# Optimization experiments

Measured on AMD Instinct MI355X. Metric: run time of the kernel, lower is better.

The kernel has to match this reference:

```python
import jax, jax.numpy as jnp
import numpy as np

N = 100000
E = 3200000
IN_C, HID, OUT_C = 512, 256, 40
NUM_LAYERS = 2
BN_EPS = 1e-5


def setup_inputs() -> dict:
    key = jax.random.key(0)
    ks = jax.random.split(key, 12)
    s = 0.05  # weight scale to keep activations sane
    return {
        "x": jax.random.normal(ks[0], (N, IN_C), jnp.float32),
        "edge_index": jax.random.randint(ks[1], (2, E), 0, N, jnp.int64),
        "fc0_W": jax.random.normal(ks[2], (IN_C, HID), jnp.float32) * s,
        "fc0_b": jax.random.normal(ks[3], (HID,), jnp.float32) * s,
        "conv_W": jax.random.normal(ks[4], (NUM_LAYERS, HID, HID), jnp.float32) * s,
        "conv_b": jax.random.normal(ks[5], (NUM_LAYERS, HID), jnp.float32) * s,
        "bn_gamma": jax.random.uniform(ks[6], (NUM_LAYERS + 1, HID), jnp.float32, 0.5, 1.5),
        "bn_beta": jax.random.normal(ks[7], (NUM_LAYERS + 1, HID), jnp.float32) * s,
        "bn_mean": jax.random.normal(ks[8], (NUM_LAYERS + 1, HID), jnp.float32) * s,
        "bn_var": jax.random.uniform(ks[9], (NUM_LAYERS + 1, HID), jnp.float32, 0.5, 1.5),
        "clf_W": jax.random.normal(ks[10], (HID, OUT_C), jnp.float32) * s,
        "clf_b": jax.random.normal(ks[11], (OUT_C,), jnp.float32) * s,
    }


def _bn(x, gamma, beta, mean, var):
    # BatchNorm1d in eval mode (running stats)
    return (x - mean) * (gamma * jax.lax.rsqrt(var + BN_EPS)) + beta


def _aggregate(x, row, col):
    # degree-normalized SpMM: out[col[e]] += (1/sqrt(d[col[e]]d[row[e]])) * x[row[e]]
    n = x.shape[0]
    d = jax.ops.segment_sum(jnp.ones((row.shape[0],), x.dtype), col, num_segments=n)
    dn = jnp.where(d > 0, jax.lax.rsqrt(d), 0.0)  # nan_to_num of 1/sqrt(0)
    val = dn[col] * dn[row]  # [E]
    msgs = val[:, None] * x[row]  # [E, HID]
    return jax.ops.segment_sum(msgs, col, num_segments=n)


def reference(x, edge_index, fc0_W, fc0_b, conv_W, conv_b,
              bn_gamma, bn_beta, bn_mean, bn_var, clf_W, clf_b):
    row, col = edge_index[0], edge_index[1]
    h = jax.nn.relu(_bn(x @ fc0_W + fc0_b, bn_gamma[0], bn_beta[0], bn_mean[0], bn_var[0]))
    prev = h  # layer_[-1] == layer_[0] (only one append)
    for i in range(NUM_LAYERS):
        h = _aggregate(h, row, col) @ conv_W[i] + conv_b[i]
        h = jax.nn.relu(_bn(h, bn_gamma[i + 1], bn_beta[i + 1], bn_mean[i + 1], bn_var[i + 1]))
        h = h + prev  # residual to first-layer features
    return h @ clf_W + clf_b
```

## Files before the change

kernel.cpp:

```cpp
#include <hip/hip_runtime.h>
#include <stdint.h>

#define NN 100000
#define NE 3200000
#define KIN 512
#define HID 256
#define NOUT 40
#define NB2 1024
#define BSHIFT2 7
#define NBKT 782
#define EPB 8192

typedef __attribute__((ext_vector_type(8))) __bf16 bf16x8;
typedef __attribute__((ext_vector_type(4))) float f32x4;

__device__ __forceinline__ float b2f(unsigned short u) {
  union { unsigned int i; float f; } x; x.i = ((unsigned int)u) << 16; return x.f;
}
__device__ __forceinline__ unsigned short f2b(float f) {
  unsigned int i = __float_as_uint(f);
  return (unsigned short)((i + 0x7FFFu + ((i >> 16) & 1u)) >> 16);
}
__device__ __forceinline__ float uf(unsigned int x) { return __uint_as_float(x); }
__device__ __forceinline__ unsigned char f2e8(float v) {
  v = fminf(v, 480.f);
  unsigned int ui = __float_as_uint(v);
  ui += 0x3FFFFu + ((ui >> 19) & 1u);
  unsigned int e32 = ui >> 23;
  if (e32 <= 120u) return 0;
  return (unsigned char)(((e32 - 120u) << 4) | ((ui >> 19) & 15u));
}
__device__ __forceinline__ float e82f(unsigned char u) {
  return __uint_as_float(((unsigned int)u) << 19) * 0x1p120f;
}
__device__ __forceinline__ unsigned short e82b(unsigned char u) {
  return u ? (unsigned short)(((unsigned int)u << 3) + 0x3C00u) : (unsigned short)0;
}
__device__ __forceinline__ unsigned short* swz(unsigned short* base, int row, int kk) {
  int byte = (row * 64 + kk * 2) ^ ((row & 7) << 4);
  return (unsigned short*)((char*)base + byte);
}
__device__ __forceinline__ char* swzst(unsigned short* base, int row, int cb) {
  int byte = (row * 128 + cb) ^ ((row & 7) << 4);
  return (char*)base + byte;
}

__global__ __launch_bounds__(256) void k_bhist(const int* __restrict__ ecol, int* __restrict__ bcnt) {
  __shared__ int hist[NB2];
  int t = threadIdx.x;
  for (int j = t; j < NB2; j += 256) hist[j] = 0;
  __syncthreads();
  int e0 = blockIdx.x * EPB, e1 = min(e0 + EPB, NE);
  for (int e = e0 + t; e < e1; e += 256) atomicAdd(&hist[ecol[e] >> BSHIFT2], 1);
  __syncthreads();
  for (int j = t; j < NB2; j += 256) if (hist[j]) atomicAdd(&bcnt[j], hist[j]);
}

__global__ void k_bscan(const int* __restrict__ bcnt, int* __restrict__ bbase, int* __restrict__ cursor) {
  __shared__ int wsum[4];
  int t = threadIdx.x, lane = t & 63, w = t >> 6;
  int4 v = *(const int4*)(bcnt + 4 * t);
  int tot = v.x + v.y + v.z + v.w;
  int s = tot;
  for (int d = 1; d < 64; d <<= 1) { int o = __shfl_up(s, d, 64); if (lane >= d) s += o; }
  if (lane == 63) wsum[w] = s;
  __syncthreads();
  int add = 0;
  for (int i = 0; i < 4; ++i) add += (i < w) ? wsum[i] : 0;
  int excl = add + s - tot;
  int p0 = excl, p1 = p0 + v.x, p2 = p1 + v.y, p3 = p2 + v.z;
  bbase[4 * t] = p0; bbase[4 * t + 1] = p1; bbase[4 * t + 2] = p2; bbase[4 * t + 3] = p3;
  cursor[4 * t] = p0; cursor[4 * t + 1] = p1; cursor[4 * t + 2] = p2; cursor[4 * t + 3] = p3;
}

__global__ __launch_bounds__(256) void k_bucket(const int* __restrict__ erow, const int* __restrict__ ecol,
                                                int* __restrict__ cursor, unsigned int* __restrict__ ebuf) {
  __shared__ int hist[NB2];
  __shared__ int base[NB2];
  int t = threadIdx.x;
  for (int j = t; j < NB2; j += 256) hist[j] = 0;
  __syncthreads();
  int e0 = blockIdx.x * EPB, e1 = min(e0 + EPB, NE);
  for (int e = e0 + t; e < e1; e += 256) atomicAdd(&hist[ecol[e] >> BSHIFT2], 1);
  __syncthreads();
  for (int j = t; j < NB2; j += 256) {
    int c = hist[j];
    base[j] = (c > 0) ? atomicAdd(&cursor[j], c) : 0;
    hist[j] = 0;
  }
  __syncthreads();
  for (int e = e0 + t; e < e1; e += 256) {
    int col = ecol[e];
    int b = col >> BSHIFT2;
    int r = atomicAdd(&hist[b], 1);
    ebuf[(size_t)base[b] + r] = ((unsigned int)(col & 127) << 17) | (unsigned int)erow[e];
  }
}

__global__ __launch_bounds__(256) void k_subdeg(const unsigned int* __restrict__ ebuf,
                                                const int* __restrict__ bbase, const int* __restrict__ bcnt,
                                                int* __restrict__ deg, float* __restrict__ dn) {
  __shared__ int h[128];
  int t = threadIdx.x, b = blockIdx.x;
  if (t < 128) h[t] = 0;
  __syncthreads();
  int s = bbase[b], e = s + bcnt[b];
  for (int i = s + t; i < e; i += 256) atomicAdd(&h[ebuf[i] >> 17], 1);
  __syncthreads();
  if (t < 128) {
    int col = (b << BSHIFT2) + t;
    if (col < NN) { int d = h[t]; deg[col] = d; dn[col] = d > 0 ? rsqrtf((float)d) : 0.f; }
  }
}

#define SCAN_CH 1024
__global__ void k_scan_part(const int* __restrict__ deg, int* __restrict__ partials) {
  __shared__ int lds[4];
  int b = blockIdx.x, t = threadIdx.x;
  int base = b * SCAN_CH;
  int s = 0;
  for (int j = 0; j < 4; ++j) { int i = base + t + 256 * j; if (i < NN) s += deg[i]; }
  for (int d = 32; d > 0; d >>= 1) s += __shfl_down(s, d, 64);
  int lane = t & 63, w = t >> 6;
  if (lane == 0) lds[w] = s;
  __syncthreads();
  if (t == 0) partials[b] = lds[0] + lds[1] + lds[2] + lds[3];
}

__global__ void k_scan_partials(int* __restrict__ partials, int nb) {
  __shared__ int lds[2];
  int t = threadIdx.x;
  int v = (t < nb) ? partials[t] : 0;
  int lane = t & 63, w = t >> 6;
  int s = v;
  for (int d = 1; d < 64; d <<= 1) { int o = __shfl_up(s, d, 64); if (lane >= d) s += o; }
  if (lane == 63) lds[w] = s;
  __syncthreads();
  int base = (w == 1) ? lds[0] : 0;
  if (t < nb) partials[t] = base + s - v;
}

__global__ void k_scan_final(const int* __restrict__ deg, const int* __restrict__ partials,
                             int* __restrict__ colptr, int* __restrict__ pos) {
  __shared__ int lds[4];
  int b = blockIdx.x, t = threadIdx.x;
  int base = b * SCAN_CH + t * 4;
  int d0 = (base + 0 < NN) ? deg[base + 0] : 0;
  int d1 = (base + 1 < NN) ? deg[base + 1] : 0;
  int d2 = (base + 2 < NN) ? deg[base + 2] : 0;
  int d3 = (base + 3 < NN) ? deg[base + 3] : 0;
  int tot = d0 + d1 + d2 + d3;
  int lane = t & 63, w = t >> 6;
  int s = tot;
  for (int d = 1; d < 64; d <<= 1) { int o = __shfl_up(s, d, 64); if (lane >= d) s += o; }
  if (lane == 63) lds[w] = s;
  __syncthreads();
  int wbase = 0;
  for (int i = 0; i < 4; ++i) wbase += (i < w) ? lds[i] : 0;
  int excl = wbase + s - tot + partials[b];
  int p0 = excl, p1 = p0 + d0, p2 = p1 + d1, p3 = p2 + d2, p4 = p3 + d3;
  if (base + 0 <= NN) colptr[base + 0] = p0;
  if (base + 1 <= NN) colptr[base + 1] = p1;
  if (base + 2 <= NN) colptr[base + 2] = p2;
  if (base + 3 <= NN) colptr[base + 3] = p3;
  if (base + 4 == NN) colptr[NN] = p4;
  if (base + 0 < NN) pos[base + 0] = p0;
  if (base + 1 < NN) pos[base + 1] = p1;
  if (base + 2 < NN) pos[base + 2] = p2;
  if (base + 3 < NN) pos[base + 3] = p3;
}

__global__ __launch_bounds__(256) void k_fill2(const unsigned int* __restrict__ ebuf,
                                               const int* __restrict__ bbase, const int* __restrict__ bcnt,
                                               int* __restrict__ pos, int* __restrict__ csr_row) {
  int b = blockIdx.x >> 2, sub = blockIdx.x & 3;
  int s = bbase[b], e = s + bcnt[b];
  int cb = b << BSHIFT2;
  for (int i = s + sub * 256 + threadIdx.x; i < e; i += 1024) {
    unsigned int pk = ebuf[i];
    int p = atomicAdd(&pos[cb | (int)(pk >> 17)], 1);
    csr_row[p] = (int)(pk & 0x1FFFF);
  }
}

__global__ void k_prep(const float* __restrict__ fc0_W, const float* __restrict__ fc0_b,
                       const float* __restrict__ conv_W, const float* __restrict__ conv_b,
                       const float* __restrict__ bn_gamma, const float* __restrict__ bn_beta,
                       const float* __restrict__ bn_mean, const float* __restrict__ bn_var,
                       const float* __restrict__ clf_W,
                       unsigned short* __restrict__ W0t, unsigned short* __restrict__ Wct,
                       unsigned short* __restrict__ Wclft,
                       float* __restrict__ epia, float* __restrict__ epib,
                       unsigned char* __restrict__ h0s) {
  int idx = blockIdx.x * 256 + threadIdx.x;
  if (idx < 131072) {
    int n = idx >> 9, k = idx & 511;
    W0t[idx] = f2b(fc0_W[k * 256 + n]);
  } else if (idx < 262144) {
    int j = idx - 131072;
    int l = j >> 16, rem = j & 65535, n = rem >> 8, k = rem & 255;
    Wct[j] = f2b(conv_W[l * 65536 + k * 256 + n]);
  } else if (idx < 262144 + 48 * 256) {
    int j = idx - 262144;
    int n = j >> 8, k = j & 255;
    Wclft[j] = f2b(n < NOUT ? clf_W[k * NOUT + n] : 0.f);
  } else if (idx < 262144 + 12288 + 768) {
    int j = idx - 262144 - 12288;
    int layer = j >> 8, c = j & 255;
    float a = bn_gamma[j] * rsqrtf(bn_var[j] + 1e-5f);
    float bias = (layer == 0) ? fc0_b[c] : conv_b[(layer - 1) * 256 + c];
    epia[j] = a;
    epib[j] = bn_beta[j] + (bias - bn_mean[j]) * a;
  } else if (idx < 262144 + 12288 + 768 + 256) {
    int c = idx - (262144 + 12288 + 768);
    h0s[(size_t)NN * HID + c] = 0;
  }
}

template <int K, int ALAY, int EPI>
__global__ __launch_bounds__(512) void k_gemm2(const void* __restrict__ Av,
                                               const unsigned short* __restrict__ Bt,
                                               const float* __restrict__ epia,
                                               const float* __restrict__ epib,
                                               const void* prevv,
                                               const float* __restrict__ dnp,
                                               const unsigned short* __restrict__ clfW,
                                               const float* __restrict__ clfb,
                                               void* outv, void* outv2) {
  __shared__ unsigned short ldsA[128 * 32];
  __shared__ unsigned short ldsB[256 * 32];
  constexpr bool DOCLF = (EPI == 0 || EPI == 4);
  const int t = threadIdx.x;
  const int w = t >> 6, lane = t & 63;
  const int lo = lane & 15, hi = lane >> 4;
  const int wr = w >> 1, wc = w & 1;
  const int m0 = blockIdx.x * 128;
  constexpr int NK = K / 32;
  f32x4 acc[2][8];
#pragma unroll
  for (int m = 0; m < 2; ++m)
#pragma unroll
    for (int f = 0; f < 8; ++f) acc[m][f] = (f32x4){0.f, 0.f, 0.f, 0.f};
  f32x4 accclf[3];
#pragma unroll
  for (int f = 0; f < 3; ++f) accclf[f] = (f32x4){0.f, 0.f, 0.f, 0.f};

  const int arow = t >> 2;
  const int akk = (t & 3) * 8;
  const int rg = m0 + arow;
  const int bn0 = t >> 2, bn1 = bn0 + 128;

  float4 rv0, rv1;
  int4 ra;
  uint2 rae;

#define LOADG(k0_) {                                                        \
    if (ALAY == 0) {                                                        \
      const float* A = (const float*)Av;                                    \
      rv0 = (float4){0.f, 0.f, 0.f, 0.f}; rv1 = rv0;                        \
      if (rg < NN) {                                                        \
        rv0 = *(const float4*)(A + (size_t)rg * K + (k0_) + akk);           \
        rv1 = *(const float4*)(A + (size_t)rg * K + (k0_) + akk + 4);       \
      }                                                                     \
    } else if (ALAY == 1) {                                                 \
      const unsigned short* A = (const unsigned short*)Av;                  \
      ra = (int4){0, 0, 0, 0};                                              \
      if (rg < NN) ra = *(const int4*)(A + (size_t)rg * K + (k0_) + akk);   \
    } else {                                                                \
      const unsigned char* A = (const unsigned char*)Av;                    \
      rae = (uint2){0u, 0u};                                                \
      if (rg < NN) rae = *(const uint2*)(A + (size_t)rg * K + (k0_) + akk); \
    }                                                                       \
    rb0 = *(const int4*)(Bt + (size_t)bn0 * K + (k0_) + akk);               \
    rb1 = *(const int4*)(Bt + (size_t)bn1 * K + (k0_) + akk);               \
  }
#define WRITELDS() {                                                        \
    if (ALAY == 0) {                                                        \
      union { unsigned short u[8]; int4 v; } pk;                            \
      pk.u[0] = f2b(rv0.x); pk.u[1] = f2b(rv0.y);                           \
      pk.u[2] = f2b(rv0.z); pk.u[3] = f2b(rv0.w);                           \
      pk.u[4] = f2b(rv1.x); pk.u[5] = f2b(rv1.y);                           \
      pk.u[6] = f2b(rv1.z); pk.u[7] = f2b(rv1.w);                           \
      *(int4*)(void*)swz(ldsA, arow, akk) = pk.v;                           \
    } else if (ALAY == 1) {                                                 \
      *(int4*)(void*)swz(ldsA, arow, akk) = ra;                             \
    } else {                                                                \
      union { unsigned char b[8]; uint2 v2; } in; in.v2 = rae;              \
      union { unsigned short u[8]; int4 v; } pk;                            \
      _Pragma("unroll") for (int q = 0; q < 8; ++q) pk.u[q] = e82b(in.b[q]);\
      *(int4*)(void*)swz(ldsA, arow, akk) = pk.v;                           \
    }                                                                       \
    *(int4*)(void*)swz(ldsB, bn0, akk) = rb0;                               \
    *(int4*)(void*)swz(ldsB, bn1, akk) = rb1;                               \
  }

  int4 rb0, rb1;
  LOADG(0);
  for (int k = 0; k < NK; ++k) {
    asm volatile("s_waitcnt lgkmcnt(0)" ::: "memory");
    __builtin_amdgcn_s_barrier();
    __builtin_amdgcn_sched_barrier(0);
    WRITELDS();
    __syncthreads();
    if (k + 1 < NK) LOADG((k + 1) * 32);
    bf16x8 af0 = *(const bf16x8*)(void*)swz(ldsA, wr * 32 + lo, hi * 8);
    bf16x8 af1 = *(const bf16x8*)(void*)swz(ldsA, wr * 32 + 16 + lo, hi * 8);
#pragma unroll
    for (int f = 0; f < 8; ++f) {
      bf16x8 bf = *(const bf16x8*)(void*)swz(ldsB, wc * 128 + f * 16 + lo, hi * 8);
      acc[0][f] = __builtin_amdgcn_mfma_f32_16x16x32_bf16(af0, bf, acc[0][f], 0, 0, 0);
      acc[1][f] = __builtin_amdgcn_mfma_f32_16x16x32_bf16(af1, bf, acc[1][f], 0, 0, 0);
    }
  }
  asm volatile("s_waitcnt lgkmcnt(0)" ::: "memory");
  __builtin_amdgcn_s_barrier();
  __builtin_amdgcn_sched_barrier(0);

#pragma unroll
  for (int cc = 0; cc < 4; ++cc) {
    if (cc) __syncthreads();
    if (wc == (cc >> 1)) {
#pragma unroll
      for (int m = 0; m < 2; ++m) {
        const int rb = wr * 32 + m * 16 + hi * 4;
#pragma unroll
        for (int fl = 0; fl < 4; ++fl) {
          const int f = (cc & 1) * 4 + fl;
          const int c = wc * 128 + f * 16 + lo;
          float a_ = epia[c], b_ = epib[c];
#pragma unroll
          for (int j = 0; j < 4; ++j) {
            int row = rb + j;
            int r = m0 + row;
            float y = fmaxf(a_ * acc[m][f][j] + b_, 0.f);
            float sv;
            if constexpr (EPI == 1) {
              float dnv = (r < NN) ? dnp[r] : 0.f;
              sv = y * dnv;
            } else {
              sv = y;
            }
            *(unsigned short*)swzst(ldsB, row, (fl * 16 + lo) * 2) = f2b(sv);
          }
        }
      }
    }
    __syncthreads();
    if constexpr (EPI == 0 || EPI == 1) {
#pragma unroll
      for (int pass = 0; pass < 2; ++pass) {
        int rr = pass * 64 + (t >> 3);
        int r = m0 + rr;
        int cb = (t & 7) * 16;
        uint4 v = *(const uint4*)swzst(ldsB, rr, cb);
        if (r < NN) {
          size_t gix = (size_t)r * HID + cc * 64 + (t & 7) * 8;
          union { unsigned short u[8]; uint4 v4; } sb; sb.v4 = v;
          if constexpr (EPI == 0) {
            float d = dnp[r];
            union { unsigned char b[8]; uint2 v2; } o8;
#pragma unroll
            for (int q = 0; q < 8; ++q) o8.b[q] = f2e8(d * b2f(sb.u[q]));
            *(uint2*)((unsigned char*)outv2 + gix) = o8.v2;
          } else {
            union { unsigned char b[8]; uint2 v2; } pv;
            pv.v2 = *(const uint2*)((const unsigned char*)prevv + gix);
            union { unsigned char b[8]; uint2 v2; } o8;
#pragma unroll
            for (int q = 0; q < 8; ++q) o8.b[q] = f2e8(b2f(sb.u[q]) + e82f(pv.b[q]));
            *(uint2*)((unsigned char*)outv + gix) = o8.v2;
          }
        }
      }
    }
    if constexpr (DOCLF) {
#pragma unroll
      for (int kk = 0; kk < 2; ++kk) {
        bf16x8 af = *(const bf16x8*)(const void*)swzst(ldsB, w * 16 + lo, (kk * 32 + hi * 8) * 2);
#pragma unroll
        for (int f = 0; f < 3; ++f) {
          bf16x8 bf = *(const bf16x8*)(clfW + (size_t)(f * 16 + lo) * HID + cc * 64 + kk * 32 + hi * 8);
          accclf[f] = __builtin_amdgcn_mfma_f32_16x16x32_bf16(af, bf, accclf[f], 0, 0, 0);
        }
      }
    }
  }
  if constexpr (DOCLF) {
#pragma unroll
    for (int f = 0; f < 3; ++f) {
      int c = f * 16 + lo;
      if (c < NOUT) {
#pragma unroll
        for (int j = 0; j < 4; ++j) {
          int r = m0 + w * 16 + hi * 4 + j;
          if (r < NN) {
            if constexpr (EPI == 0) {
              ((float*)outv)[(size_t)r * NOUT + c] = accclf[f][j];
            } else {
              ((float*)outv)[(size_t)r * NOUT + c] =
                  accclf[f][j] + ((const float*)prevv)[(size_t)r * NOUT + c] + clfb[c];
            }
          }
        }
      }
    }
  }
#undef LOADG
#undef WRITELDS
}

__global__ __launch_bounds__(256) void k_agg(const int* __restrict__ colptr,
                                             const int* __restrict__ csr,
                                             const float* __restrict__ dn,
                                             const unsigned char* __restrict__ hs,
                                             unsigned char* __restrict__ X) {
  int w = threadIdx.x >> 6, lane = threadIdx.x & 63;
  int i = blockIdx.x * 4 + w;
  int hl = lane & 31, half = lane >> 5;
  const unsigned char* hb = hs + hl * 8;
  int e0 = colptr[i], e1 = colptr[i + 1];
  float a0 = 0, a1 = 0, a2 = 0, a3 = 0, a4 = 0, a5 = 0, a6 = 0, a7 = 0;
  int rA[4], rB[4];
  uint2 vA[4], vB[4];

#define LOADIDX(e_, r_) { \
  _Pragma("unroll") for (int u = 0; u < 4; ++u) { \
    int ee = (e_) + 2 * u + half; \
    int rr = csr[ee]; \
    r_[u] = (ee < e1) ? rr : NN; } }
#define GATHER(r_, v_) { \
  _Pragma("unroll") for (int u = 0; u < 4; ++u) \
    v_[u] = *(const uint2*)(hb + (size_t)r_[u] * HID); }
#define ACCUM(v_) { \
  _Pragma("unroll") for (int u = 0; u < 4; ++u) { \
    a0 += uf((v_[u].x << 19) & 0x07F80000u); a1 += uf((v_[u].x << 11) & 0x07F80000u); \
    a2 += uf((v_[u].x << 3)  & 0x07F80000u); a3 += uf((v_[u].x >> 5)  & 0x07F80000u); \
    a4 += uf((v_[u].y << 19) & 0x07F80000u); a5 += uf((v_[u].y << 11) & 0x07F80000u); \
    a6 += uf((v_[u].y << 3)  & 0x07F80000u); a7 += uf((v_[u].y >> 5)  & 0x07F80000u); } }

  int nb = (e1 - e0 + 7) >> 3;
  if (nb == 1) {
    LOADIDX(e0, rA); GATHER(rA, vA); ACCUM(vA);
  } else if (nb > 1) {
    LOADIDX(e0, rA);
    GATHER(rA, vA);
    LOADIDX(e0 + 8, rB);
    int b = 1, e = e0 + 8;
    for (; b + 1 < nb; ++b, e += 8) {
      if (b & 1) { GATHER(rB, vB); LOADIDX(e + 8, rA); ACCUM(vA); }
      else       { GATHER(rA, vA); LOADIDX(e + 8, rB); ACCUM(vB); }
    }
    if (b & 1) { GATHER(rB, vB); ACCUM(vA); ACCUM(vB); }
    else       { GATHER(rA, vA); ACCUM(vB); ACCUM(vA); }
  }
  a0 += __shfl_xor(a0, 32); a1 += __shfl_xor(a1, 32);
  a2 += __shfl_xor(a2, 32); a3 += __shfl_xor(a3, 32);
  a4 += __shfl_xor(a4, 32); a5 += __shfl_xor(a5, 32);
  a6 += __shfl_xor(a6, 32); a7 += __shfl_xor(a7, 32);
  if (half == 0) {
    float d = dn[i] * 0x1p120f;
    union { unsigned char b[8]; uint2 v; } o;
    o.b[0] = f2e8(d * a0); o.b[1] = f2e8(d * a1); o.b[2] = f2e8(d * a2); o.b[3] = f2e8(d * a3);
    o.b[4] = f2e8(d * a4); o.b[5] = f2e8(d * a5); o.b[6] = f2e8(d * a6); o.b[7] = f2e8(d * a7);
    *(uint2*)(X + (size_t)i * HID + hl * 8) = o.v;
  }
}

extern "C" void kernel_launch(void* const* d_in, const int* in_sizes, int n_in,
                              void* d_out, int out_size, void* d_ws, size_t ws_size,
                              hipStream_t stream) {
  const float* x        = (const float*)d_in[0];
  const int*   edge     = (const int*)d_in[1];
  const int*   erow     = edge;
  const int*   ecol     = edge + NE;
  const float* fc0_W    = (const float*)d_in[2];
  const float* fc0_b    = (const float*)d_in[3];
  const float* conv_W   = (const float*)d_in[4];
  const float* conv_b   = (const float*)d_in[5];
  const float* bn_gamma = (const float*)d_in[6];
  const float* bn_beta  = (const float*)d_in[7];
  const float* bn_mean  = (const float*)d_in[8];
  const float* bn_var   = (const float*)d_in[9];
  const float* clf_W    = (const float*)d_in[10];
  const float* clf_b    = (const float*)d_in[11];

  char* p = (char*)d_ws;
  auto alloc = [&](size_t bytes) { char* r = p; p += (bytes + 255) & ~(size_t)255; return r; };
  int*   deg      = (int*)alloc((size_t)NN * 4);
  float* dn       = (float*)alloc((size_t)NN * 4);
  int*   colptr   = (int*)alloc((size_t)(NN + 1) * 4);
  int*   pos      = (int*)alloc((size_t)NN * 4);
  int*   partials = (int*)alloc(1024);
  int*   bcnt     = (int*)alloc(NB2 * 4);
  int*   bbase    = (int*)alloc(NB2 * 4);
  int*   cursor   = (int*)alloc(NB2 * 4);
  int*   csr_row  = (int*)alloc(((size_t)NE + 16) * 4);
  unsigned short* W0t   = (unsigned short*)alloc((size_t)256 * 512 * 2);
  unsigned short* Wct   = (unsigned short*)alloc((size_t)2 * 256 * 256 * 2);
  unsigned short* Wclft = (unsigned short*)alloc((size_t)48 * 256 * 2);
  float* epia = (float*)alloc(768 * 4);
  float* epib = (float*)alloc(768 * 4);
  float* outP = (float*)alloc((size_t)NN * NOUT * 4);
  unsigned char*  h0s = (unsigned char*)alloc((size_t)(NN + 1) * HID);
  unsigned char*  X   = (unsigned char*)alloc((size_t)NN * HID);
  unsigned int* ebuf = (unsigned int*)X;

  int nbBlk = (NE + EPB - 1) / EPB;
  hipMemsetAsync(bcnt, 0, NB2 * 4, stream);
  k_bhist<<<nbBlk, 256, 0, stream>>>(ecol, bcnt);
  k_bscan<<<1, 256, 0, stream>>>(bcnt, bbase, cursor);
  k_bucket<<<nbBlk, 256, 0, stream>>>(erow, ecol, cursor, ebuf);
  k_subdeg<<<NBKT, 256, 0, stream>>>(ebuf, bbase, bcnt, deg, dn);
  int nb = (NN + SCAN_CH - 1) / SCAN_CH;
  k_scan_part<<<nb, 256, 0, stream>>>(deg, partials);
  k_scan_partials<<<1, 128, 0, stream>>>(partials, nb);
  k_scan_final<<<nb, 256, 0, stream>>>(deg, partials, colptr, pos);
  k_fill2<<<NBKT * 4, 256, 0, stream>>>(ebuf, bbase, bcnt, pos, csr_row);
  k_prep<<<1076, 256, 0, stream>>>(fc0_W, fc0_b, conv_W, conv_b, bn_gamma, bn_beta,
                                   bn_mean, bn_var, clf_W, W0t, Wct, Wclft, epia, epib, h0s);

  int gm2 = (NN + 127) / 128;
  k_gemm2<KIN, 0, 0><<<gm2, 512, 0, stream>>>(x, W0t, epia, epib, nullptr, dn, Wclft, nullptr, outP, h0s);
  k_agg<<<(NN + 3) / 4, 256, 0, stream>>>(colptr, csr_row, dn, h0s, X);
  k_gemm2<HID, 2, 1><<<gm2, 512, 0, stream>>>(X, Wct, epia + 256, epib + 256, h0s, dn, nullptr, nullptr, h0s, nullptr);
  k_agg<<<(NN + 3) / 4, 256, 0, stream>>>(colptr, csr_row, dn, h0s, X);
  k_gemm2<HID, 2, 4><<<gm2, 512, 0, stream>>>(X, Wct + 65536, epia + 512, epib + 512, outP, nullptr, Wclft, clf_b, d_out, nullptr);
}
```

Baseline: 622.7 us.

## Load GEMM operands straight from global memory into MFMA fragments, dropping LDS staging

The GEMM main loop no longer stages A and B tiles through shared memory with barriers and prefetch registers. Each wave now reads its own A fragments (fp32 or e8 converted to bf16) and B fragments directly from global memory, relying on L1/L2 caching. One shared buffer is kept only for the epilogue staging. This removes LDS write/read traffic and per-k barriers, but B is re-read by every wave and the loads are less coalesced, with no software prefetch. The ALAY==1 bf16 path is also dropped, and any instantiation with ALAY==1 would now read A as uint8.

```diff
diff --git a/kernel.cpp b/kernel.cpp
--- a/kernel.cpp
+++ b/kernel.cpp
@@ -36,13 +36,13 @@
 __device__ __forceinline__ unsigned short e82b(unsigned char u) {
   return u ? (unsigned short)(((unsigned int)u << 3) + 0x3C00u) : (unsigned short)0;
 }
+__device__ __forceinline__ char* swzst(unsigned short* base, int row, int cb) {
+  int byte = (row * 128 + cb) ^ ((row & 7) << 4);
+  return (char*)base + byte;
+}
 __device__ __forceinline__ unsigned short* swz(unsigned short* base, int row, int kk) {
   int byte = (row * 64 + kk * 2) ^ ((row & 7) << 4);
   return (unsigned short*)((char*)base + byte);
-}
-__device__ __forceinline__ char* swzst(unsigned short* base, int row, int cb) {
-  int byte = (row * 128 + cb) ^ ((row & 7) << 4);
-  return (char*)base + byte;
 }
 
 __global__ __launch_bounds__(256) void k_bhist(const int* __restrict__ ecol, int* __restrict__ bcnt) {
@@ -227,8 +227,7 @@
                                                const unsigned short* __restrict__ clfW,
                                                const float* __restrict__ clfb,
                                                void* outv, void* outv2) {
-  __shared__ unsigned short ldsA[128 * 32];
-  __shared__ unsigned short ldsB[256 * 32];
+  __shared__ unsigned short stg[128 * 64];
   constexpr bool DOCLF = (EPI == 0 || EPI == 4);
   const int t = threadIdx.x;
   const int w = t >> 6, lane = t & 63;
@@ -245,76 +244,49 @@
 #pragma unroll
   for (int f = 0; f < 3; ++f) accclf[f] = (f32x4){0.f, 0.f, 0.f, 0.f};
 
-  const int arow = t >> 2;
-  const int akk = (t & 3) * 8;
-  const int rg = m0 + arow;
-  const int bn0 = t >> 2, bn1 = bn0 + 128;
-
-  float4 rv0, rv1;
-  int4 ra;
-  uint2 rae;
-
-#define LOADG(k0_) {                                                        \
-    if (ALAY == 0) {                                                        \
-      const float* A = (const float*)Av;                                    \
-      rv0 = (float4){0.f, 0.f, 0.f, 0.f}; rv1 = rv0;                        \
-      if (rg < NN) {                                                        \
-        rv0 = *(const float4*)(A + (size_t)rg * K + (k0_) + akk);           \
-        rv1 = *(const float4*)(A + (size_t)rg * K + (k0_) + akk + 4);       \
-      }                                                                     \
-    } else if (ALAY == 1) {                                                 \
-      const unsigned short* A = (const unsigned short*)Av;                  \
-      ra = (int4){0, 0, 0, 0};                                              \
-      if (rg < NN) ra = *(const int4*)(A + (size_t)rg * K + (k0_) + akk);   \
-    } else {                                                                \
-      const unsigned char* A = (const unsigned char*)Av;                    \
-      rae = (uint2){0u, 0u};                                                \
-      if (rg < NN) rae = *(const uint2*)(A + (size_t)rg * K + (k0_) + akk); \
-    }                                                                       \
-    rb0 = *(const int4*)(Bt + (size_t)bn0 * K + (k0_) + akk);               \
-    rb1 = *(const int4*)(Bt + (size_t)bn1 * K + (k0_) + akk);               \
-  }
-#define WRITELDS() {                                                        \
-    if (ALAY == 0) {                                                        \
-      union { unsigned short u[8]; int4 v; } pk;                            \
-      pk.u[0] = f2b(rv0.x); pk.u[1] = f2b(rv0.y);                           \
-      pk.u[2] = f2b(rv0.z); pk.u[3] = f2b(rv0.w);                           \
-      pk.u[4] = f2b(rv1.x); pk.u[5] = f2b(rv1.y);                           \
-      pk.u[6] = f2b(rv1.z); pk.u[7] = f2b(rv1.w);                           \
-      *(int4*)(void*)swz(ldsA, arow, akk) = pk.v;                           \
-    } else if (ALAY == 1) {                                                 \
-      *(int4*)(void*)swz(ldsA, arow, akk) = ra;                             \
-    } else {                                                                \
-      union { unsigned char b[8]; uint2 v2; } in; in.v2 = rae;              \
-      union { unsigned short u[8]; int4 v; } pk;                            \
-      _Pragma("unroll") for (int q = 0; q < 8; ++q) pk.u[q] = e82b(in.b[q]);\
-      *(int4*)(void*)swz(ldsA, arow, akk) = pk.v;                           \
-    }                                                                       \
-    *(int4*)(void*)swz(ldsB, bn0, akk) = rb0;                               \
-    *(int4*)(void*)swz(ldsB, bn1, akk) = rb1;                               \
-  }
-
-  int4 rb0, rb1;
-  LOADG(0);
+  const int r0 = m0 + wr * 32 + lo;
+  const int r1 = r0 + 16;
+  const int bn = wc * 128 + lo;
+
   for (int k = 0; k < NK; ++k) {
-    asm volatile("s_waitcnt lgkmcnt(0)" ::: "memory");
-    __builtin_amdgcn_s_barrier();
-    __builtin_amdgcn_sched_barrier(0);
-    WRITELDS();
-    __syncthreads();
-    if (k + 1 < NK) LOADG((k + 1) * 32);
-    bf16x8 af0 = *(const bf16x8*)(void*)swz(ldsA, wr * 32 + lo, hi * 8);
-    bf16x8 af1 = *(const bf16x8*)(void*)swz(ldsA, wr * 32 + 16 + lo, hi * 8);
+    const int k0 = k * 32 + hi * 8;
+    bf16x8 af0, af1;
+    if constexpr (ALAY == 0) {
+      const float* A = (const float*)Av;
+      float4 v0a = {0.f, 0.f, 0.f, 0.f}, v0b = v0a, v1a = v0a, v1b = v0a;
+      if (r0 < NN) {
+        v0a = *(const float4*)(A + (size_t)r0 * K + k0);
+        v0b = *(const float4*)(A + (size_t)r0 * K + k0 + 4);
+      }
+      if (r1 < NN) {
+        v1a = *(const float4*)(A + (size_t)r1 * K + k0);
+        v1b = *(const float4*)(A + (size_t)r1 * K + k0 + 4);
+      }
+      union { unsigned short u[8]; bf16x8 v; } p0, p1;
+      p0.u[0] = f2b(v0a.x); p0.u[1] = f2b(v0a.y); p0.u[2] = f2b(v0a.z); p0.u[3] = f2b(v0a.w);
+      p0.u[4] = f2b(v0b.x); p0.u[5] = f2b(v0b.y); p0.u[6] = f2b(v0b.z); p0.u[7] = f2b(v0b.w);
+      p1.u[0] = f2b(v1a.x); p1.u[1] = f2b(v1a.y); p1.u[2] = f2b(v1a.z); p1.u[3] = f2b(v1a.w);
+      p1.u[4] = f2b(v1b.x); p1.u[5] = f2b(v1b.y); p1.u[6] = f2b(v1b.z); p1.u[7] = f2b(v1b.w);
+      af0 = p0.v; af1 = p1.v;
+    } else {
+      const unsigned char* A = (const unsigned char*)Av;
+      uint2 u0 = {0u, 0u}, u1 = {0u, 0u};
+      if (r0 < NN) u0 = *(const uint2*)(A + (size_t)r0 * K + k0);
+      if (r1 < NN) u1 = *(const uint2*)(A + (size_t)r1 * K + k0);
+      union { unsigned char b[8]; uint2 v; } i0, i1;
+      i0.v = u0; i1.v = u1;
+      union { unsigned short u[8]; bf16x8 v; } p0, p1;
+#pragma unroll
+      for (int q = 0; q < 8; ++q) { p0.u[q] = e82b(i0.b[q]); p1.u[q] = e82b(i1.b[q]); }
+      af0 = p0.v; af1 = p1.v;
+    }
 #pragma unroll
     for (int f = 0; f < 8; ++f) {
-      bf16x8 bf = *(const bf16x8*)(void*)swz(ldsB, wc * 128 + f * 16 + lo, hi * 8);
+      bf16x8 bf = *(const bf16x8*)(Bt + (size_t)(bn + f * 16) * K + k0);
       acc[0][f] = __builtin_amdgcn_mfma_f32_16x16x32_bf16(af0, bf, acc[0][f], 0, 0, 0);
       acc[1][f] = __builtin_amdgcn_mfma_f32_16x16x32_bf16(af1, bf, acc[1][f], 0, 0, 0);
     }
   }
-  asm volatile("s_waitcnt lgkmcnt(0)" ::: "memory");
-  __builtin_amdgcn_s_barrier();
-  __builtin_amdgcn_sched_barrier(0);
 
 #pragma unroll
   for (int cc = 0; cc < 4; ++cc) {
@@ -340,7 +312,7 @@
             } else {
               sv = y;
             }
-            *(unsigned short*)swzst(ldsB, row, (fl * 16 + lo) * 2) = f2b(sv);
+            *(unsigned short*)swzst(stg, row, (fl * 16 + lo) * 2) = f2b(sv);
           }
         }
       }
@@ -352,7 +324,7 @@
         int rr = pass * 64 + (t >> 3);
         int r = m0 + rr;
         int cb = (t & 7) * 16;
-        uint4 v = *(const uint4*)swzst(ldsB, rr, cb);
+        uint4 v = *(const uint4*)swzst(stg, rr, cb);
         if (r < NN) {
           size_t gix = (size_t)r * HID + cc * 64 + (t & 7) * 8;
           union { unsigned short u[8]; uint4 v4; } sb; sb.v4 = v;
@@ -376,7 +348,7 @@
     if constexpr (DOCLF) {
 #pragma unroll
       for (int kk = 0; kk < 2; ++kk) {
-        bf16x8 af = *(const bf16x8*)(const void*)swzst(ldsB, w * 16 + lo, (kk * 32 + hi * 8) * 2);
+        bf16x8 af = *(const bf16x8*)(const void*)swzst(stg, w * 16 + lo, (kk * 32 + hi * 8) * 2);
 #pragma unroll
         for (int f = 0; f < 3; ++f) {
           bf16x8 bf = *(const bf16x8*)(clfW + (size_t)(f * 16 + lo) * HID + cc * 64 + kk * 32 + hi * 8);
@@ -405,8 +377,6 @@
       }
     }
   }
-#undef LOADG
-#undef WRITELDS
 }
 
 __global__ __launch_bounds__(256) void k_agg(const int* __restrict__ colptr,
```

Result: slower. 832.9 us (+33.8%).
